# Performance work log

Hardware: AMD Instinct MI355X
Metric: run time of the kernel (lower is better)

## Reference

```python
import jax, jax.numpy as jnp
import numpy as np

N_NODES = 100000
N_EDGES = 1600000
IN_FEATS = 512
OUT_FEATS = 128


def setup_inputs() -> dict:
    key = jax.random.key(0)
    k1, k2, k3, k4, k5 = jax.random.split(key, 5)
    feat = jax.random.normal(k1, (N_NODES, IN_FEATS), dtype=jnp.float32)
    src = jax.random.randint(k2, (N_EDGES,), 0, N_NODES, dtype=jnp.int32)
    dst = jax.random.randint(k3, (N_EDGES,), 0, N_NODES, dtype=jnp.int32)
    edge_weight = jax.random.uniform(k4, (N_EDGES,), dtype=jnp.float32)
    # xavier_uniform init for the [in, out] weight
    limit = float(np.sqrt(6.0 / (IN_FEATS + OUT_FEATS)))
    weight = jax.random.uniform(k5, (IN_FEATS, OUT_FEATS), dtype=jnp.float32,
                                minval=-limit, maxval=limit)
    bias = jnp.zeros((OUT_FEATS,), dtype=jnp.float32)
    return {"feat": feat, "weight": weight, "bias": bias,
            "edge_weight": edge_weight, "src": src, "dst": dst}


def reference(feat, weight, bias, edge_weight, src, dst):
    n = feat.shape[0]
    ones = jnp.ones_like(edge_weight)
    # degrees from edge list; clamp(min=1)
    out_deg = jnp.maximum(jax.ops.segment_sum(ones, src, num_segments=n), 1.0)
    in_deg = jnp.maximum(jax.ops.segment_sum(ones, dst, num_segments=n), 1.0)
    # norm='both': left-normalize source feats by out_deg^-0.5
    feat_src = feat * jax.lax.rsqrt(out_deg)[:, None]
    # in_feats > out_feats -> project before aggregation
    h = feat_src @ weight                      # [N, OUT]
    msg = h[src] * edge_weight[:, None]        # u_mul_e, [E, OUT]
    rst = jax.ops.segment_sum(msg, dst, num_segments=n)  # fn.sum per dst
    # right-normalize by in_deg^-0.5, add bias (activation is None)
    rst = rst * jax.lax.rsqrt(in_deg)[:, None] + bias
    return rst
```

## Files before the change

### kernel.cpp

```cpp
#include <hip/hip_runtime.h>
#include <hip/hip_bf16.h>

#define NNODES 100000
#define NEDGES 1600000
#define INF 512
#define OUTF 128
#define NB 391
#define BCAP 5120
#define SEG 2048
#define BK 32
#define NKSTEP (INF / BK)

typedef __attribute__((ext_vector_type(8))) __bf16 bf16x8;
typedef __attribute__((ext_vector_type(4))) float f32x4;

typedef const __attribute__((address_space(1))) unsigned int* gas_ptr;
typedef __attribute__((address_space(3))) unsigned int* las_ptr;

__device__ __forceinline__ void gload_lds16(const void* g, void* l) {
  __builtin_amdgcn_global_load_lds((gas_ptr)g, (las_ptr)l, 16, 0, 0);
}

__global__ void wt_kernel(const float* __restrict__ w, unsigned short* __restrict__ wta) {
  int i = blockIdx.x * blockDim.x + threadIdx.x;
  if (i >= 8192) return;
  int lane = i & 63;
  int c8   = (i >> 6) & 7;
  int kb   = i >> 9;
  int n = c8 * 16 + (lane & 15);
  int kbase = kb * 32 + (lane >> 4) * 8;
  unsigned short tmp[8];
#pragma unroll
  for (int j = 0; j < 8; ++j) {
    __bf16 b = (__bf16)(w[(size_t)(kbase + j) * OUTF + n]);
    tmp[j] = __builtin_bit_cast(unsigned short, b);
  }
  ((int4*)wta)[i] = *(int4*)tmp;
}

__global__ __launch_bounds__(256) void bucket_kernel(
    const int* __restrict__ src, const int* __restrict__ dst,
    const float* __restrict__ ew, int* __restrict__ out_cnt,
    int* __restrict__ bucket_cnt, int2* __restrict__ bucket) {
  __shared__ int hist[NB];
  __shared__ int base[NB];
  int t = threadIdx.x;
  for (int i = t; i < NB; i += 256) hist[i] = 0;
  __syncthreads();
  int e0 = blockIdx.x * SEG;
  int e1 = min(e0 + SEG, NEDGES);
  for (int e = e0 + t; e < e1; e += 256) {
    atomicAdd(&out_cnt[src[e]], 1);
    atomicAdd(&hist[dst[e] >> 8], 1);
  }
  __syncthreads();
  for (int i = t; i < NB; i += 256) {
    int c = hist[i];
    base[i] = c ? atomicAdd(&bucket_cnt[i], c) : 0;
    hist[i] = 0;
  }
  __syncthreads();
  for (int e = e0 + t; e < e1; e += 256) {
    int d = dst[e];
    int b = d >> 8;
    int r = atomicAdd(&hist[b], 1);
    int2 en;
    en.x = ((d & 255) << 17) | src[e];
    en.y = __float_as_int(ew[e]);
    bucket[(size_t)b * BCAP + base[b] + r] = en;
  }
}

__global__ __launch_bounds__(512) void bscan_kernel(const int* __restrict__ bucket_cnt,
                                                    int* __restrict__ bucket_base,
                                                    int* __restrict__ rowptr) {
  __shared__ int s[512];
  int t = threadIdx.x;
  int v = (t < NB) ? bucket_cnt[t] : 0;
  s[t] = v;
  __syncthreads();
  for (int off = 1; off < 512; off <<= 1) {
    int x = (t >= off) ? s[t - off] : 0;
    __syncthreads();
    s[t] += x;
    __syncthreads();
  }
  if (t < NB) bucket_base[t] = s[t] - v;
  if (t == 0) rowptr[NNODES] = NEDGES;
}

__global__ __launch_bounds__(256) void csr_kernel(
    const int* __restrict__ bucket_cnt, const int* __restrict__ bucket_base,
    const int2* __restrict__ bucket, int* __restrict__ rowptr,
    int2* __restrict__ epair) {
  __shared__ int hist[256];
  __shared__ int cur[256];
  int b = blockIdx.x;
  int t = threadIdx.x;
  int nb = bucket_cnt[b];
  int bbase = bucket_base[b];
  const int2* bk = bucket + (size_t)b * BCAP;
  hist[t] = 0;
  __syncthreads();
  for (int i = t; i < nb; i += 256) atomicAdd(&hist[bk[i].x >> 17], 1);
  __syncthreads();
  int v = hist[t];
  for (int off = 1; off < 256; off <<= 1) {
    int x = (t >= off) ? hist[t - off] : 0;
    __syncthreads();
    hist[t] += x;
    __syncthreads();
  }
  int excl = hist[t] - v;
  int node = b * 256 + t;
  if (node < NNODES) rowptr[node] = bbase + excl;
  cur[t] = excl;
  __syncthreads();
  for (int i = t; i < nb; i += 256) {
    int2 en = bk[i];
    int nl = en.x >> 17;
    int r = atomicAdd(&cur[nl], 1);
    epair[bbase + r] = make_int2(en.x & 0x1FFFF, en.y);
  }
}

__global__ __launch_bounds__(256, 4) void gemm_kernel(
    const float* __restrict__ feat, const unsigned short* __restrict__ wta,
    const int* __restrict__ out_cnt, unsigned short* __restrict__ h) {
  __shared__ float As[2][64 * BK];
  __shared__ unsigned short Bs[2][4096];

  const int t = threadIdx.x;
  const int lane = t & 63;
  const int wave = t >> 6;
  const int l15 = lane & 15;
  const int lg  = lane >> 4;
  const int rowbase = blockIdx.x * 64;

  const int srow_off = lane >> 3;
  const int schunk = (lane & 7) ^ srow_off;

  const int row = min(rowbase + wave * 16 + l15, NNODES - 1);
  const float s0 = rsqrtf(fmaxf((float)out_cnt[row], 1.0f));

  f32x4 acc[8];
#pragma unroll
  for (int c = 0; c < 8; ++c) acc[c] = (f32x4){0.f, 0.f, 0.f, 0.f};

#define STAGE(buf, kb)                                                         \
  {                                                                            \
    _Pragma("unroll")                                                          \
    for (int q = 0; q < 2; ++q) {                                              \
      int i = wave * 2 + q;                                                    \
      int gr = min(rowbase + i * 8 + srow_off, NNODES - 1);                    \
      const float* ga = feat + (size_t)gr * INF + (kb) * BK + schunk * 4;      \
      gload_lds16(ga, &As[buf][i * 256]);                                      \
      const unsigned short* gb =                                               \
          wta + (size_t)(kb) * 4096 + i * 512 + lane * 8;                      \
      gload_lds16(gb, &Bs[buf][i * 512]);                                      \
    }                                                                          \
  }

  int buf = 0;
  STAGE(0, 0);
  __syncthreads();

  for (int kb = 0; kb < NKSTEP; ++kb) {
    if (kb + 1 < NKSTEP) STAGE(buf ^ 1, kb + 1);

    bf16x8 bfr[8];
#pragma unroll
    for (int c = 0; c < 8; ++c)
      bfr[c] = *(const bf16x8*)&Bs[buf][c * 512 + lane * 8];

    int r = wave * 16 + l15;
    int c0 = (lg * 2) ^ (l15 & 7);
    int c1 = (lg * 2 + 1) ^ (l15 & 7);
    f32x4 u = *(const f32x4*)&As[buf][r * 32 + c0 * 4];
    f32x4 v = *(const f32x4*)&As[buf][r * 32 + c1 * 4];
    bf16x8 a;
#pragma unroll
    for (int j = 0; j < 4; ++j) {
      a[j]     = (__bf16)(u[j] * s0);
      a[j + 4] = (__bf16)(v[j] * s0);
    }

#pragma unroll
    for (int c = 0; c < 8; ++c)
      acc[c] = __builtin_amdgcn_mfma_f32_16x16x32_bf16(a, bfr[c], acc[c], 0, 0, 0);

    __syncthreads();
    buf ^= 1;
  }
#undef STAGE

  int rb = rowbase + wave * 16 + lg * 4;
#pragma unroll
  for (int r = 0; r < 4; ++r) {
    int orow = rb + r;
    if (orow < NNODES) {
#pragma unroll
      for (int c = 0; c < 8; ++c) {
        __bf16 bv = (__bf16)acc[c][r];
        h[(size_t)orow * OUTF + c * 16 + l15] = __builtin_bit_cast(unsigned short, bv);
      }
    }
  }
}

__device__ __forceinline__ float blo(unsigned int u) { return __uint_as_float(u << 16); }
__device__ __forceinline__ float bhi(unsigned int u) { return __uint_as_float(u & 0xFFFF0000u); }

__global__ __launch_bounds__(256) void gather_kernel(
    const int* __restrict__ rowptr, const int2* __restrict__ epair,
    const unsigned short* __restrict__ h, const float* __restrict__ bias,
    float* __restrict__ out) {
  const int lane = threadIdx.x & 63;
  const int half = lane >> 5;
  const int grp  = (lane >> 4) & 1;
  const int li   = lane & 15;
  const int wid  = (blockIdx.x * blockDim.x + threadIdx.x) >> 6;
  const int nw   = (gridDim.x * blockDim.x) >> 6;

  for (int p = wid; p < NNODES / 2; p += nw) {
    const int node = p * 2 + half;
    const int beg = rowptr[node];
    const int end = rowptr[node + 1];

    float a0 = 0.f, a1 = 0.f, a2 = 0.f, a3 = 0.f;
    float a4 = 0.f, a5 = 0.f, a6 = 0.f, a7 = 0.f;

    int e = beg + grp;
#define GSTEP(pr)                                                              \
      {                                                                        \
        const unsigned int* hp =                                               \
            (const unsigned int*)(h + (size_t)(pr).x * OUTF) + li * 4;         \
        uint4 u = *(const uint4*)hp;                                           \
        float w = __int_as_float((pr).y);                                      \
        a0 += blo(u.x) * w; a1 += bhi(u.x) * w;                                \
        a2 += blo(u.y) * w; a3 += bhi(u.y) * w;                                \
        a4 += blo(u.z) * w; a5 += bhi(u.z) * w;                                \
        a6 += blo(u.w) * w; a7 += bhi(u.w) * w;                                \
      }
    for (; e + 14 < end; e += 16) {
      int2 p0 = epair[e];
      int2 p1 = epair[e + 2];
      int2 p2 = epair[e + 4];
      int2 p3 = epair[e + 6];
      int2 p4 = epair[e + 8];
      int2 p5 = epair[e + 10];
      int2 p6 = epair[e + 12];
      int2 p7 = epair[e + 14];
      GSTEP(p0); GSTEP(p1); GSTEP(p2); GSTEP(p3);
      GSTEP(p4); GSTEP(p5); GSTEP(p6); GSTEP(p7);
    }
    for (; e + 6 < end; e += 8) {
      int2 p0 = epair[e];
      int2 p1 = epair[e + 2];
      int2 p2 = epair[e + 4];
      int2 p3 = epair[e + 6];
      GSTEP(p0); GSTEP(p1); GSTEP(p2); GSTEP(p3);
    }
    for (; e < end; e += 2) {
      int2 pr = epair[e];
      GSTEP(pr);
    }
#undef GSTEP

    a0 += __shfl_xor(a0, 16); a1 += __shfl_xor(a1, 16);
    a2 += __shfl_xor(a2, 16); a3 += __shfl_xor(a3, 16);
    a4 += __shfl_xor(a4, 16); a5 += __shfl_xor(a5, 16);
    a6 += __shfl_xor(a6, 16); a7 += __shfl_xor(a7, 16);

    if (grp == 0) {
      float sc = rsqrtf(fmaxf((float)(end - beg), 1.0f));
      f32x4 b0 = ((const f32x4*)bias)[li * 2];
      f32x4 b1 = ((const f32x4*)bias)[li * 2 + 1];
      f32x4 v0, v1;
      v0.x = a0 * sc + b0.x; v0.y = a1 * sc + b0.y;
      v0.z = a2 * sc + b0.z; v0.w = a3 * sc + b0.w;
      v1.x = a4 * sc + b1.x; v1.y = a5 * sc + b1.y;
      v1.z = a6 * sc + b1.z; v1.w = a7 * sc + b1.w;
      f32x4* op = (f32x4*)(out + (size_t)node * OUTF);
      op[li * 2] = v0;
      op[li * 2 + 1] = v1;
    }
  }
}

extern "C" void kernel_launch(void* const* d_in, const int* in_sizes, int n_in,
                              void* d_out, int out_size, void* d_ws, size_t ws_size,
                              hipStream_t stream) {
  const float* feat   = (const float*)d_in[0];
  const float* weight = (const float*)d_in[1];
  const float* bias   = (const float*)d_in[2];
  const float* ew     = (const float*)d_in[3];
  const int*   src    = (const int*)d_in[4];
  const int*   dst    = (const int*)d_in[5];
  float* out = (float*)d_out;
  char* ws = (char*)d_ws;

  int* out_cnt        = (int*)ws;
  int* rowptr         = (int*)(ws + 0x80000);
  int* bucket_cnt     = (int*)(ws + 0x100000);
  int* bucket_base    = (int*)(ws + 0x101000);
  unsigned short* wta = (unsigned short*)(ws + 0x110000);
  int2* bucket        = (int2*)(ws + 0x140000);
  int2* epair         = (int2*)(ws + 0x1200000);
  unsigned short* h   = (unsigned short*)(ws + 0x2000000);

  hipMemsetAsync(out_cnt, 0, NNODES * sizeof(int), stream);
  hipMemsetAsync(bucket_cnt, 0, NB * sizeof(int), stream);

  wt_kernel<<<32, 256, 0, stream>>>(weight, wta);
  bucket_kernel<<<(NEDGES + SEG - 1) / SEG, 256, 0, stream>>>(src, dst, ew, out_cnt,
                                                              bucket_cnt, bucket);
  bscan_kernel<<<1, 512, 0, stream>>>(bucket_cnt, bucket_base, rowptr);
  csr_kernel<<<NB, 256, 0, stream>>>(bucket_cnt, bucket_base, bucket, rowptr, epair);
  gemm_kernel<<<(NNODES + 63) / 64, 256, 0, stream>>>(feat, wta, out_cnt, h);
  gather_kernel<<<2048, 256, 0, stream>>>(rowptr, epair, h, bias, out);
}
```

Baseline: 259.9 us.

## Double GEMM K-tile to 64 and drop 16-edge unroll in gather loop

The GEMM K tile grows from 32 to 64, so the kernel runs 8 pipeline stages with half as many barriers. The A tile gets a new 16-chunk XOR swizzle and the B tile is now read from LDS per k-substep. Launch bounds drop to 2 blocks per CU because LDS use doubles, which may reduce occupancy and latency hiding. The gather kernel also loses its 8-edge unrolled loop, falling back to the 4-edge unroll, which lowers register pressure but leaves fewer loads in flight.

```diff
diff --git a/kernel.cpp b/kernel.cpp
--- a/kernel.cpp
+++ b/kernel.cpp
@@ -8,8 +8,8 @@
 #define NB 391
 #define BCAP 5120
 #define SEG 2048
-#define BK 32
-#define NKSTEP (INF / BK)
+#define BK2 64
+#define NK2 (INF / BK2)
 
 typedef __attribute__((ext_vector_type(8))) __bf16 bf16x8;
 typedef __attribute__((ext_vector_type(4))) float f32x4;
@@ -124,11 +124,11 @@
   }
 }
 
-__global__ __launch_bounds__(256, 4) void gemm_kernel(
+__global__ __launch_bounds__(256, 2) void gemm_kernel(
     const float* __restrict__ feat, const unsigned short* __restrict__ wta,
     const int* __restrict__ out_cnt, unsigned short* __restrict__ h) {
-  __shared__ float As[2][64 * BK];
-  __shared__ unsigned short Bs[2][4096];
+  __shared__ float As[2][64 * BK2];
+  __shared__ unsigned short Bs[2][8192];
 
   const int t = threadIdx.x;
   const int lane = t & 63;
@@ -137,8 +137,8 @@
   const int lg  = lane >> 4;
   const int rowbase = blockIdx.x * 64;
 
-  const int srow_off = lane >> 3;
-  const int schunk = (lane & 7) ^ srow_off;
+  const int r4 = lane >> 4;
+  const int ch = lane & 15;
 
   const int row = min(rowbase + wave * 16 + l15, NNODES - 1);
   const float s0 = rsqrtf(fmaxf((float)out_cnt[row], 1.0f));
@@ -147,17 +147,23 @@
 #pragma unroll
   for (int c = 0; c < 8; ++c) acc[c] = (f32x4){0.f, 0.f, 0.f, 0.f};
 
-#define STAGE(buf, kb)                                                         \
+#define STAGE(buf, s)                                                          \
   {                                                                            \
     _Pragma("unroll")                                                          \
-    for (int q = 0; q < 2; ++q) {                                              \
-      int i = wave * 2 + q;                                                    \
-      int gr = min(rowbase + i * 8 + srow_off, NNODES - 1);                    \
-      const float* ga = feat + (size_t)gr * INF + (kb) * BK + schunk * 4;      \
+    for (int q = 0; q < 4; ++q) {                                              \
+      int i = wave * 4 + q;                                                    \
+      int lrow = 4 * i + r4;                                                   \
+      int gr = min(rowbase + lrow, NNODES - 1);                                \
+      int lc = ch ^ (lrow & 15);                                               \
+      const float* ga = feat + (size_t)gr * INF + (s) * BK2 + lc * 4;          \
       gload_lds16(ga, &As[buf][i * 256]);                                      \
+    }                                                                          \
+    _Pragma("unroll")                                                          \
+    for (int q = 0; q < 4; ++q) {                                              \
+      int j = wave * 4 + q;                                                    \
       const unsigned short* gb =                                               \
-          wta + (size_t)(kb) * 4096 + i * 512 + lane * 8;                      \
-      gload_lds16(gb, &Bs[buf][i * 512]);                                      \
+          wta + (size_t)(s) * 8192 + j * 512 + lane * 8;                       \
+      gload_lds16(gb, &Bs[buf][j * 512]);                                      \
     }                                                                          \
   }
 
@@ -165,29 +171,27 @@
   STAGE(0, 0);
   __syncthreads();
 
-  for (int kb = 0; kb < NKSTEP; ++kb) {
-    if (kb + 1 < NKSTEP) STAGE(buf ^ 1, kb + 1);
-
-    bf16x8 bfr[8];
-#pragma unroll
-    for (int c = 0; c < 8; ++c)
-      bfr[c] = *(const bf16x8*)&Bs[buf][c * 512 + lane * 8];
-
-    int r = wave * 16 + l15;
-    int c0 = (lg * 2) ^ (l15 & 7);
-    int c1 = (lg * 2 + 1) ^ (l15 & 7);
-    f32x4 u = *(const f32x4*)&As[buf][r * 32 + c0 * 4];
-    f32x4 v = *(const f32x4*)&As[buf][r * 32 + c1 * 4];
-    bf16x8 a;
-#pragma unroll
-    for (int j = 0; j < 4; ++j) {
-      a[j]     = (__bf16)(u[j] * s0);
-      a[j + 4] = (__bf16)(v[j] * s0);
-    }
-
-#pragma unroll
-    for (int c = 0; c < 8; ++c)
-      acc[c] = __builtin_amdgcn_mfma_f32_16x16x32_bf16(a, bfr[c], acc[c], 0, 0, 0);
+  for (int s = 0; s < NK2; ++s) {
+    if (s + 1 < NK2) STAGE(buf ^ 1, s + 1);
+
+    const int r = wave * 16 + l15;
+#pragma unroll
+    for (int kk = 0; kk < 2; ++kk) {
+      int lc0 = kk * 8 + lg * 2;
+      f32x4 u = *(const f32x4*)&As[buf][r * BK2 + ((lc0) ^ l15) * 4];
+      f32x4 v = *(const f32x4*)&As[buf][r * BK2 + ((lc0 + 1) ^ l15) * 4];
+      bf16x8 a;
+#pragma unroll
+      for (int j = 0; j < 4; ++j) {
+        a[j]     = (__bf16)(u[j] * s0);
+        a[j + 4] = (__bf16)(v[j] * s0);
+      }
+#pragma unroll
+      for (int c = 0; c < 8; ++c) {
+        bf16x8 b = *(const bf16x8*)&Bs[buf][kk * 4096 + c * 512 + lane * 8];
+        acc[c] = __builtin_amdgcn_mfma_f32_16x16x32_bf16(a, b, acc[c], 0, 0, 0);
+      }
+    }
 
     __syncthreads();
     buf ^= 1;
@@ -242,18 +246,6 @@
         a4 += blo(u.z) * w; a5 += bhi(u.z) * w;                                \
         a6 += blo(u.w) * w; a7 += bhi(u.w) * w;                                \
       }
-    for (; e + 14 < end; e += 16) {
-      int2 p0 = epair[e];
-      int2 p1 = epair[e + 2];
-      int2 p2 = epair[e + 4];
-      int2 p3 = epair[e + 6];
-      int2 p4 = epair[e + 8];
-      int2 p5 = epair[e + 10];
-      int2 p6 = epair[e + 12];
-      int2 p7 = epair[e + 14];
-      GSTEP(p0); GSTEP(p1); GSTEP(p2); GSTEP(p3);
-      GSTEP(p4); GSTEP(p5); GSTEP(p6); GSTEP(p7);
-    }
     for (; e + 6 < end; e += 8) {
       int2 p0 = epair[e];
       int2 p1 = epair[e + 2];
```

Measured after the change: 271.0 us. +4.3%, slower.
